# Performance work log

Measured on AMD Instinct MI355X. Metric: run time of the kernel, lower is better.

The kernel has to match this reference:

```python
import jax, jax.numpy as jnp
import numpy as np

# dims
D_MODEL = 256; D_STATE = 16; D_CONV = 4; EXPAND = 2
D_INNER = D_MODEL * EXPAND            # 512
DT_RANK = 16                          # ceil(256/16)
B_SZ = 16; C_IN = 64; T_LR = 2560; R = 2; C_OUT = 64


def _p(key, shape, scale=0.02):
    return jax.random.normal(key, shape, jnp.float32) * scale


def setup_inputs() -> dict:
    key = jax.random.key(0)
    ks = iter(jax.random.split(key, 48))
    inp = {}
    inp['x'] = jax.random.normal(next(ks), (B_SZ, C_IN, T_LR), jnp.float32)
    # encoder: Conv1d(64->128,k3,p1) ; Conv1d(128->256,k3,p1)
    inp['enc_w1'] = _p(next(ks), (128, C_IN, 3)); inp['enc_b1'] = jnp.zeros((128,), jnp.float32)
    inp['enc_w2'] = _p(next(ks), (256, 128, 3)); inp['enc_b2'] = jnp.zeros((256,), jnp.float32)
    # BidirectionalMamba norms
    inp['norm1_w'] = jnp.ones((D_MODEL,), jnp.float32)
    inp['norm2_w'] = jnp.ones((D_MODEL,), jnp.float32)
    # one forward ('f') and one backward ('b') Mamba v1 block
    for p in ('f', 'b'):
        inp[p + '_inW'] = _p(next(ks), (2 * D_INNER, D_MODEL))
        inp[p + '_convW'] = _p(next(ks), (D_INNER, D_CONV), 0.2)
        inp[p + '_convb'] = jnp.zeros((D_INNER,), jnp.float32)
        inp[p + '_xW'] = _p(next(ks), (DT_RANK + 2 * D_STATE, D_INNER))
        inp[p + '_dtW'] = _p(next(ks), (D_INNER, DT_RANK), 0.1)
        inp[p + '_dtb'] = -4.0 + 2.0 * jax.random.uniform(next(ks), (D_INNER,), jnp.float32)
        inp[p + '_Alog'] = jnp.log(jnp.tile(jnp.arange(1, D_STATE + 1, dtype=jnp.float32), (D_INNER, 1)))
        inp[p + '_D'] = jnp.ones((D_INNER,), jnp.float32)
        inp[p + '_outW'] = _p(next(ks), (D_MODEL, D_INNER))
    # post-bottleneck: Conv1d(512->256,k3,p1) + BatchNorm1d(256) (eval)
    inp['convd_w'] = _p(next(ks), (256, 512, 3)); inp['convd_b'] = jnp.zeros((256,), jnp.float32)
    inp['bn_g'] = jnp.ones((256,), jnp.float32); inp['bn_b'] = jnp.zeros((256,), jnp.float32)
    inp['bn_mean'] = jnp.zeros((256,), jnp.float32); inp['bn_var'] = jnp.ones((256,), jnp.float32)
    # SubPixel1D: Conv1d(256 -> target_channels*r, k3, p1), r=2
    inp['sp_w'] = _p(next(ks), (C_OUT * R, 256, 3)); inp['sp_b'] = jnp.zeros((C_OUT * R,), jnp.float32)
    return inp


def silu(x):
    return x * jax.nn.sigmoid(x)


def conv1d(x, w, b):  # x: (B,C,L), w: (O,I,K), 'same' padding
    k = w.shape[-1]
    y = jax.lax.conv_general_dilated(x, w, (1,), [(k // 2, k // 2)],
                                     dimension_numbers=('NCH', 'OIH', 'NCH'))
    return y + b[None, :, None]


def rmsnorm(x, w, eps=1e-6):
    return x * jax.lax.rsqrt(jnp.mean(x * x, -1, keepdims=True) + eps) * w


def mamba(x, inW, convW, convb, xW, dtW, dtb, Alog, Dp, outW):
    # x: (B, L, D_MODEL) -> (B, L, D_MODEL); Mamba v1 selective scan.
    Bn = x.shape[0]
    xz = x @ inW.T                               # (B,L,2*di)
    xc, z = jnp.split(xz, 2, axis=-1)            # (B,L,di) each
    # causal depthwise conv over time
    xt = jnp.transpose(xc, (0, 2, 1))            # (B,di,L)
    xt = jax.lax.conv_general_dilated(xt, convW[:, None, :], (1,), [(D_CONV - 1, 0)],
                                      dimension_numbers=('NCH', 'OIH', 'NCH'),
                                      feature_group_count=D_INNER)
    xc = silu(jnp.transpose(xt + convb[None, :, None], (0, 2, 1)))  # (B,L,di)
    dbc = xc @ xW.T                              # (B,L,dt_rank+2N)
    dt = jax.nn.softplus(dbc[..., :DT_RANK] @ dtW.T + dtb)          # (B,L,di)
    Bc = dbc[..., DT_RANK:DT_RANK + D_STATE]     # (B,L,N)
    Cc = dbc[..., DT_RANK + D_STATE:]            # (B,L,N)
    A = -jnp.exp(Alog)                           # (di,N)

    def step(h, inp):
        dt_t, B_t, C_t, x_t = inp                # (B,di),(B,N),(B,N),(B,di)
        dA = jnp.exp(dt_t[..., None] * A)        # (B,di,N)
        h = dA * h + (dt_t * x_t)[..., None] * B_t[:, None, :]
        y = jnp.einsum('bdn,bn->bd', h, C_t)
        return h, y

    xs = (jnp.transpose(dt, (1, 0, 2)), jnp.transpose(Bc, (1, 0, 2)),
          jnp.transpose(Cc, (1, 0, 2)), jnp.transpose(xc, (1, 0, 2)))
    h0 = jnp.zeros((Bn, D_INNER, D_STATE), x.dtype)
    _, ys = jax.lax.scan(step, h0, xs)           # ys: (L,B,di)
    y = jnp.transpose(ys, (1, 0, 2)) + xc * Dp
    return (y * silu(z)) @ outW.T


def reference(x, enc_w1, enc_b1, enc_w2, enc_b2, norm1_w, norm2_w,
              f_inW, f_convW, f_convb, f_xW, f_dtW, f_dtb, f_Alog, f_D, f_outW,
              b_inW, b_convW, b_convb, b_xW, b_dtW, b_dtb, b_Alog, b_D, b_outW,
              convd_w, convd_b, bn_g, bn_b, bn_mean, bn_var, sp_w, sp_b):
    # encoder (dropout = identity in eval)
    e = silu(conv1d(x, enc_w1, enc_b1))
    e = silu(conv1d(e, enc_w2, enc_b2))          # (B,256,T)
    t = jnp.transpose(e, (0, 2, 1))              # (B,T,256)
    # Bi-Mamba bottleneck layer
    xn = rmsnorm(t, norm1_w)
    mo_f = mamba(xn, f_inW, f_convW, f_convb, f_xW, f_dtW, f_dtb, f_Alog, f_D, f_outW) + xn
    xb = xn[:, ::-1, :]
    mo_b = mamba(xb, b_inW, b_convW, b_convb, b_xW, b_dtW, b_dtb, b_Alog, b_D, b_outW) + xb
    mo_b = mo_b[:, ::-1, :]
    combined = rmsnorm(mo_f + mo_b, norm2_w)
    m = jnp.concatenate([combined, t], axis=-1)  # (B,T,512)
    m = jnp.transpose(m, (0, 2, 1))              # (B,512,T)
    # conv_d + BatchNorm1d (eval) + SiLU
    d = conv1d(m, convd_w, convd_b)
    d = (d - bn_mean[None, :, None]) * jax.lax.rsqrt(bn_var + 1e-5)[None, :, None] \
        * bn_g[None, :, None] + bn_b[None, :, None]
    d = silu(d)
    # SubPixel1D upsample x2
    s = conv1d(d, sp_w, sp_b)                    # (B, C_OUT*R, T)
    Bn, C, T = s.shape
    s = s.reshape(Bn, C // R, R, T).transpose(0, 1, 3, 2).reshape(Bn, C // R, T * R)
    return s                                      # (B, 64, 5120)
```

## Files before the change

kernel.cpp:

```cpp
#include <hip/hip_runtime.h>
#include <hip/hip_bf16.h>
#include <math.h>

#define B_SZ 16
#define T_LR 2560
#define BT (B_SZ * T_LR)
#define DM 256
#define DI 512
#define DS 16
#define DTR 16
#define CH 128
#define CH_LOG2 7
#define CLEN (T_LR / CH)

typedef __attribute__((ext_vector_type(8))) short bf16x8;
typedef __attribute__((ext_vector_type(4))) float f32x4;

__device__ __forceinline__ float silu_f(float x) {
    return x / (1.f + __expf(-x));
}
__device__ __forceinline__ unsigned short f2bf(float v) {
    __hip_bfloat16 h = __float2bfloat16(v);
    return *(unsigned short*)&h;
}
__device__ __forceinline__ float bf2f(unsigned short u) {
    union { unsigned int i; float f; } c;
    c.i = (unsigned int)u << 16;
    return c.f;
}
__device__ __forceinline__ int seqrev(int r) {
    int s = r / T_LR, t = r % T_LR;
    return s * T_LR + (T_LR - 1 - t);
}
__device__ __forceinline__ float softplus_f(float x) {
    return (x > 20.f) ? x : __logf(1.f + __expf(x));
}

__global__ __launch_bounds__(256) void k_prep(
    const float* __restrict__ enc_w1, const float* __restrict__ enc_w2,
    const float* __restrict__ convd_w, const float* __restrict__ sp_w,
    const float* __restrict__ convd_b, const float* __restrict__ bn_g,
    const float* __restrict__ bn_b, const float* __restrict__ bn_mean,
    const float* __restrict__ bn_var,
    const float* __restrict__ inW0, const float* __restrict__ inW1,
    const float* __restrict__ outW0, const float* __restrict__ outW1,
    const float* __restrict__ xW0, const float* __restrict__ xW1,
    const float* __restrict__ Alog0, const float* __restrict__ Alog1,
    const float* __restrict__ x,
    unsigned short* __restrict__ W1r, unsigned short* __restrict__ W2r,
    unsigned short* __restrict__ Wdr, unsigned short* __restrict__ Wspr,
    float* __restrict__ alpha, float* __restrict__ beta,
    unsigned short* __restrict__ inW_bf2, unsigned short* __restrict__ outW_bf2,
    unsigned short* __restrict__ xW_bc2, float* __restrict__ Aflag,
    unsigned short* __restrict__ xt)
{
    __shared__ float ts[32][33];
    __shared__ int s_ok;
    int blk = blockIdx.x;
    int tid = threadIdx.x;
    if (blk < 32) {
        int i = blk * 256 + tid;
        int n = i / 64, ci = i % 64;
        #pragma unroll
        for (int k = 0; k < 3; k++)
            W1r[((size_t)k * 128 + n) * 64 + ci] = f2bf(enc_w1[((size_t)n * 64 + ci) * 3 + k]);
    } else if (blk < 160) {
        int i = (blk - 32) * 256 + tid;
        int n = i / 128, ci = i % 128;
        #pragma unroll
        for (int k = 0; k < 3; k++)
            W2r[((size_t)k * 256 + n) * 128 + ci] = f2bf(enc_w2[((size_t)n * 128 + ci) * 3 + k]);
    } else if (blk < 672) {
        int i = (blk - 160) * 256 + tid;
        int n = i / 512, ci = i % 512;
        #pragma unroll
        for (int k = 0; k < 3; k++)
            Wdr[((size_t)k * 256 + n) * 512 + ci] = f2bf(convd_w[((size_t)n * 512 + ci) * 3 + k]);
    } else if (blk < 800) {
        int i = (blk - 672) * 256 + tid;
        int n = i / 256, ci = i % 256;
        #pragma unroll
        for (int k = 0; k < 3; k++)
            Wspr[((size_t)k * 128 + n) * 256 + ci] = f2bf(sp_w[((size_t)n * 256 + ci) * 3 + k]);
    } else if (blk < 801) {
        int c = tid;
        float a = bn_g[c] * rsqrtf(bn_var[c] + 1e-5f);
        alpha[c] = a;
        beta[c] = (convd_b[c] - bn_mean[c]) * a + bn_b[c];
    } else if (blk < 1825) {
        int i = (blk - 801) * 256 + tid;
        inW_bf2[i] = f2bf(inW0[i]);
        inW_bf2[262144 + i] = f2bf(inW1[i]);
    } else if (blk < 2337) {
        int i = (blk - 1825) * 256 + tid;
        outW_bf2[i] = f2bf(outW0[i]);
        outW_bf2[131072 + i] = f2bf(outW1[i]);
    } else if (blk < 2433) {
        int i = (blk - 2337) * 256 + tid;
        xW_bc2[i] = f2bf(xW0[i]);
        xW_bc2[24576 + i] = f2bf(xW1[i]);
    } else if (blk < 2434) {
        if (tid == 0) s_ok = 1;
        __syncthreads();
        int ok = 1;
        for (int i = tid; i < DI * DS; i += 256) {
            int d = i >> 4, n = i & 15;
            float a0f = __expf(Alog0[d * DS]);
            float anf = __expf(Alog0[d * DS + n]);
            if (fabsf(anf - (float)(n + 1) * a0f) > 1e-3f * (float)(n + 1)) ok = 0;
            float a0b = __expf(Alog1[d * DS]);
            float anb = __expf(Alog1[d * DS + n]);
            if (fabsf(anb - (float)(n + 1) * a0b) > 1e-3f * (float)(n + 1)) ok = 0;
        }
        if (!ok) atomicAnd(&s_ok, 0);
        __syncthreads();
        if (tid == 0) Aflag[0] = s_ok ? 1.f : 0.f;
    } else {
        int idx = blk - 2434;
        int t0 = (idx % 80) * 32;
        int c0 = ((idx / 80) & 1) * 32;
        int b = idx / 160;
        int tx = tid & 31, ty = tid >> 5;
        #pragma unroll
        for (int j = 0; j < 4; j++) {
            int c = c0 + ty + j * 8;
            ts[ty + j * 8][tx] = x[((size_t)b * 64 + c) * T_LR + t0 + tx];
        }
        __syncthreads();
        #pragma unroll
        for (int j = 0; j < 4; j++) {
            int t = t0 + ty + j * 8;
            xt[((size_t)b * T_LR + t) * 64 + c0 + tx] = f2bf(ts[tx][ty + j * 8]);
        }
    }
}

__global__ __launch_bounds__(256, 4) void k_conv3_bf(const unsigned short* __restrict__ A1, int K1,
                                                  const unsigned short* __restrict__ A2, int K2,
                                                  const unsigned short* __restrict__ W,
                                                  const float* __restrict__ alpha,
                                                  const float* __restrict__ beta,
                                                  float* __restrict__ outf,
                                                  unsigned short* __restrict__ outb,
                                                  int N, int dosilu, int pixsh) {
    int Kt = K1 + K2;
    __shared__ unsigned short As[130][40];
    int tid = threadIdx.x;
    int wave = tid >> 6, lane = tid & 63;
    int wm = (wave >> 1) * 64, wn = (wave & 1) * 64;
    int m0 = blockIdx.x * 128, n0 = blockIdx.y * 128;
    int b = m0 / T_LR, t0 = m0 % T_LR;
    int q = lane >> 4, ml = lane & 15;
    const unsigned short* wbase = W + (size_t)(n0 + wn + ml) * Kt + q * 8;
    size_t tapstride = (size_t)N * Kt;
    size_t nistride  = (size_t)16 * Kt;
    f32x4 acc[4][4] = {};
    for (int k0 = 0; k0 < Kt; k0 += 32) {
        __syncthreads();
        for (int i = tid; i < 520; i += 256) {
            int row = i >> 2, cq = i & 3;
            int t = t0 - 1 + row;
            uint4 v = make_uint4(0u, 0u, 0u, 0u);
            if (t >= 0 && t < T_LR) {
                int col = k0 + cq * 8;
                const unsigned short* src = (col < K1)
                    ? A1 + (size_t)(b * T_LR + t) * K1 + col
                    : A2 + (size_t)(b * T_LR + t) * K2 + (col - K1);
                v = *(const uint4*)src;
            }
            *(uint4*)&As[row][cq * 8] = v;
        }
        __syncthreads();
        #pragma unroll
        for (int tap = 0; tap < 3; tap++) {
            bf16x8 bfr[4];
            #pragma unroll
            for (int ni = 0; ni < 4; ni++)
                bfr[ni] = *(const bf16x8*)(wbase + tap * tapstride + ni * nistride + k0);
            #pragma unroll
            for (int mi = 0; mi < 4; mi++) {
                bf16x8 af = *(const bf16x8*)&As[wm + mi * 16 + ml + tap][q * 8];
                #pragma unroll
                for (int ni = 0; ni < 4; ni++)
                    acc[mi][ni] = __builtin_amdgcn_mfma_f32_16x16x32_bf16(af, bfr[ni], acc[mi][ni], 0, 0, 0);
            }
        }
    }
    #pragma unroll
    for (int mi = 0; mi < 4; mi++) {
        #pragma unroll
        for (int r = 0; r < 4; r++) {
            int mr = m0 + wm + mi * 16 + q * 4 + r;
            int t = mr - b * T_LR;
            #pragma unroll
            for (int ni = 0; ni < 4; ni++) {
                int col = n0 + wn + ni * 16 + ml;
                float a = alpha ? alpha[col] : 1.f;
                float v = acc[mi][ni][r] * a + beta[col];
                if (dosilu) v = silu_f(v);
                if (pixsh) {
                    int c2 = col >> 1, rr = col & 1;
                    outf[(((size_t)b * 64 + c2) * T_LR + t) * 2 + rr] = v;
                } else {
                    size_t o = (size_t)mr * N + col;
                    if (outf) outf[o] = v;
                    if (outb) outb[o] = f2bf(v);
                }
            }
        }
    }
}

__global__ __launch_bounds__(256) void k_inproj_conv(const unsigned short* __restrict__ xn,
                                                     const unsigned short* __restrict__ inW,
                                                     const float* __restrict__ cw,
                                                     const float* __restrict__ cb,
                                                     unsigned short* __restrict__ xcs,
                                                     int arev) {
    __shared__ unsigned short As[128][40];
    __shared__ unsigned short Bs[128][40];
    __shared__ unsigned short Ct[131][136];
    int tid = threadIdx.x;
    int wave = tid >> 6, lane = tid & 63;
    int wm = (wave >> 1) * 64, wn = (wave & 1) * 64;
    int m0 = blockIdx.x * 128, n0 = blockIdx.y * 128;
    int b = m0 / T_LR, t0 = m0 % T_LR;
    int sc = tid & 3, sr = tid >> 2;
    int ar0 = m0 + sr, ar1 = m0 + sr + 64;
    if (arev) { ar0 = seqrev(ar0); ar1 = seqrev(ar1); }
    const unsigned short* ap0 = xn + (size_t)ar0 * DM + sc * 8;
    const unsigned short* ap1 = xn + (size_t)ar1 * DM + sc * 8;
    const unsigned short* bp0 = inW + (size_t)(n0 + sr) * DM + sc * 8;
    const unsigned short* bp1 = inW + (size_t)(n0 + sr + 64) * DM + sc * 8;
    f32x4 acc[4][4] = {};
    int q = lane >> 4, ml = lane & 15;
    for (int k0 = 0; k0 < DM; k0 += 32) {
        uint4 a0 = *(const uint4*)(ap0 + k0);
        uint4 a1 = *(const uint4*)(ap1 + k0);
        uint4 b0 = *(const uint4*)(bp0 + k0);
        uint4 b1 = *(const uint4*)(bp1 + k0);
        __syncthreads();
        *(uint4*)&As[sr][sc * 8]      = a0;
        *(uint4*)&As[sr + 64][sc * 8] = a1;
        *(uint4*)&Bs[sr][sc * 8]      = b0;
        *(uint4*)&Bs[sr + 64][sc * 8] = b1;
        __syncthreads();
        bf16x8 af[4], bfr[4];
        #pragma unroll
        for (int mi = 0; mi < 4; mi++)
            af[mi] = *(const bf16x8*)&As[wm + mi * 16 + ml][q * 8];
        #pragma unroll
        for (int ni = 0; ni < 4; ni++)
            bfr[ni] = *(const bf16x8*)&Bs[wn + ni * 16 + ml][q * 8];
        #pragma unroll
        for (int mi = 0; mi < 4; mi++)
            #pragma unroll
            for (int ni = 0; ni < 4; ni++)
                acc[mi][ni] = __builtin_amdgcn_mfma_f32_16x16x32_bf16(af[mi], bfr[ni], acc[mi][ni], 0, 0, 0);
    }
    #pragma unroll
    for (int mi = 0; mi < 4; mi++)
        #pragma unroll
        for (int r = 0; r < 4; r++)
            #pragma unroll
            for (int ni = 0; ni < 4; ni++)
                Ct[3 + wm + mi * 16 + q * 4 + r][wn + ni * 16 + ml] = f2bf(acc[mi][ni][r]);
    for (int i = tid; i < 384; i += 256) {
        int hr = i >> 7, c = i & 127;
        int tr = t0 - 3 + hr;
        float v = 0.f;
        if (tr >= 0) {
            int src = b * T_LR + (arev ? (T_LR - 1 - tr) : tr);
            const unsigned short* xr = xn + (size_t)src * DM;
            const unsigned short* wr = inW + (size_t)(n0 + c) * DM;
            for (int k = 0; k < DM; k += 8) {
                uint4 xa = *(const uint4*)(xr + k);
                uint4 wa = *(const uint4*)(wr + k);
                const unsigned short* xs = (const unsigned short*)&xa;
                const unsigned short* wsp = (const unsigned short*)&wa;
                #pragma unroll
                for (int j = 0; j < 8; j++) v += bf2f(xs[j]) * bf2f(wsp[j]);
            }
        }
        Ct[hr][c] = f2bf(v);
    }
    __syncthreads();
    int col = tid & 127;
    int d = n0 + col;
    float w0 = cw[d * 4 + 0], w1 = cw[d * 4 + 1], w2 = cw[d * 4 + 2], w3 = cw[d * 4 + 3];
    float bi = cb[d];
    int rbase = tid >> 7;
    for (int j = 0; j < 64; j++) {
        int row = rbase + 2 * j;
        float v = bi + bf2f(Ct[row][col]) * w0 + bf2f(Ct[row + 1][col]) * w1
                     + bf2f(Ct[row + 2][col]) * w2 + bf2f(Ct[row + 3][col]) * w3;
        xcs[(size_t)(m0 + row) * DI + d] = f2bf(silu_f(v));
    }
}

__global__ __launch_bounds__(256) void k_rmsnorm(const float* __restrict__ in1,
                                                 const float* __restrict__ w,
                                                 float* __restrict__ out,
                                                 unsigned short* __restrict__ out_bf,
                                                 int ntok) {
    int tok = (blockIdx.x * 256 + threadIdx.x) >> 6;
    int lane = threadIdx.x & 63;
    if (tok >= ntok) return;
    float4 v = ((const float4*)(in1 + (size_t)tok * DM))[lane];
    float ss = v.x * v.x + v.y * v.y + v.z * v.z + v.w * v.w;
    #pragma unroll
    for (int off = 32; off > 0; off >>= 1) ss += __shfl_xor(ss, off);
    float sc = rsqrtf(ss * (1.f / 256.f) + 1e-6f);
    float4 wv = ((const float4*)w)[lane];
    float4 o;
    o.x = v.x * sc * wv.x; o.y = v.y * sc * wv.y;
    o.z = v.z * sc * wv.z; o.w = v.w * sc * wv.w;
    if (out) ((float4*)(out + (size_t)tok * DM))[lane] = o;
    if (out_bf) {
        ushort4 ob;
        ob.x = f2bf(o.x); ob.y = f2bf(o.y); ob.z = f2bf(o.z); ob.w = f2bf(o.w);
        ((ushort4*)(out_bf + (size_t)tok * DM))[lane] = ob;
    }
}

__global__ __launch_bounds__(256) void k_gemm_bf(const unsigned short* __restrict__ A, int lda,
                                                 const unsigned short* __restrict__ Bw,
                                                 float* Cf, unsigned short* Cb, int ldc,
                                                 const float* __restrict__ res,
                                                 const float* __restrict__ bias,
                                                 const unsigned short* __restrict__ gate,
                                                 int K, int Nout, int act,
                                                 int arev, int crev, int accum) {
    __shared__ unsigned short As[128][40];
    __shared__ unsigned short Bs[128][40];
    int tid = threadIdx.x;
    int wave = tid >> 6, lane = tid & 63;
    int wm = (wave >> 1) * 64, wn = (wave & 1) * 64;
    int m0 = blockIdx.x * 128, n0 = blockIdx.y * 128;
    int sc = tid & 3, sr = tid >> 2;
    int ar0 = m0 + sr, ar1 = m0 + sr + 64;
    if (arev) { ar0 = seqrev(ar0); ar1 = seqrev(ar1); }
    const unsigned short* ap0 = A + (size_t)ar0 * lda + sc * 8;
    const unsigned short* ap1 = A + (size_t)ar1 * lda + sc * 8;
    bool bv0 = (n0 + sr) < Nout;
    bool bv1 = (n0 + sr + 64) < Nout;
    const unsigned short* bp0 = Bw + (size_t)(n0 + sr) * K + sc * 8;
    const unsigned short* bp1 = Bw + (size_t)(n0 + sr + 64) * K + sc * 8;
    f32x4 acc[4][4] = {};
    int q = lane >> 4, ml = lane & 15;
    for (int k0 = 0; k0 < K; k0 += 32) {
        uint4 a0 = *(const uint4*)(ap0 + k0);
        uint4 a1 = *(const uint4*)(ap1 + k0);
        uint4 b0 = make_uint4(0u, 0u, 0u, 0u), b1 = make_uint4(0u, 0u, 0u, 0u);
        if (bv0) b0 = *(const uint4*)(bp0 + k0);
        if (bv1) b1 = *(const uint4*)(bp1 + k0);
        __syncthreads();
        *(uint4*)&As[sr][sc * 8]      = a0;
        *(uint4*)&As[sr + 64][sc * 8] = a1;
        *(uint4*)&Bs[sr][sc * 8]      = b0;
        *(uint4*)&Bs[sr + 64][sc * 8] = b1;
        __syncthreads();
        bf16x8 af[4], bfr[4];
        #pragma unroll
        for (int mi = 0; mi < 4; mi++)
            af[mi] = *(const bf16x8*)&As[wm + mi * 16 + ml][q * 8];
        #pragma unroll
        for (int ni = 0; ni < 4; ni++)
            bfr[ni] = *(const bf16x8*)&Bs[wn + ni * 16 + ml][q * 8];
        #pragma unroll
        for (int mi = 0; mi < 4; mi++)
            #pragma unroll
            for (int ni = 0; ni < 4; ni++)
                acc[mi][ni] = __builtin_amdgcn_mfma_f32_16x16x32_bf16(af[mi], bfr[ni], acc[mi][ni], 0, 0, 0);
    }
    #pragma unroll
    for (int mi = 0; mi < 4; mi++) {
        #pragma unroll
        for (int r = 0; r < 4; r++) {
            int mr = m0 + wm + mi * 16 + q * 4 + r;
            int orow = crev ? seqrev(mr) : mr;
            #pragma unroll
            for (int ni = 0; ni < 4; ni++) {
                int col = n0 + wn + ni * 16 + ml;
                if (col < Nout) {
                    float v = acc[mi][ni][r];
                    if (bias) v += bias[col];
                    if (act == 2) v = softplus_f(v);
                    if (gate) v = silu_f(v) * bf2f(gate[(size_t)mr * ldc + col]);
                    if (res) v += res[(size_t)orow * ldc + col];
                    if (accum) v += Cf[(size_t)orow * ldc + col];
                    if (Cf) Cf[(size_t)orow * ldc + col] = v;
                    if (Cb) Cb[(size_t)orow * ldc + col] = f2bf(v);
                }
            }
        }
    }
}

__global__ __launch_bounds__(256) void k_gemm_bf_cb(const unsigned short* __restrict__ A, int lda,
                                                    const unsigned short* __restrict__ Bw,
                                                    unsigned short* __restrict__ Cb, int ldc,
                                                    const float* __restrict__ bias,
                                                    const unsigned short* __restrict__ gate,
                                                    int K, int act, int arev) {
    __shared__ __align__(16) unsigned short smem[2 * 128 * 40];
    unsigned short (*As)[40] = (unsigned short(*)[40])smem;
    unsigned short (*Bs)[40] = (unsigned short(*)[40])(smem + 128 * 40);
    float* sC = (float*)smem;
    int tid = threadIdx.x;
    int wave = tid >> 6, lane = tid & 63;
    int wm = (wave >> 1) * 64, wn = (wave & 1) * 64;
    int m0 = blockIdx.x * 128, n0 = blockIdx.y * 128;
    int sc = tid & 3, sr = tid >> 2;
    int ar0 = m0 + sr, ar1 = m0 + sr + 64;
    if (arev) { ar0 = seqrev(ar0); ar1 = seqrev(ar1); }
    const unsigned short* ap0 = A + (size_t)ar0 * lda + sc * 8;
    const unsigned short* ap1 = A + (size_t)ar1 * lda + sc * 8;
    const unsigned short* bp0 = Bw + (size_t)(n0 + sr) * K + sc * 8;
    const unsigned short* bp1 = Bw + (size_t)(n0 + sr + 64) * K + sc * 8;
    f32x4 acc[4][4] = {};
    int q = lane >> 4, ml = lane & 15;
    for (int k0 = 0; k0 < K; k0 += 32) {
        uint4 a0 = *(const uint4*)(ap0 + k0);
        uint4 a1 = *(const uint4*)(ap1 + k0);
        uint4 b0 = *(const uint4*)(bp0 + k0);
        uint4 b1 = *(const uint4*)(bp1 + k0);
        __syncthreads();
        *(uint4*)&As[sr][sc * 8]      = a0;
        *(uint4*)&As[sr + 64][sc * 8] = a1;
        *(uint4*)&Bs[sr][sc * 8]      = b0;
        *(uint4*)&Bs[sr + 64][sc * 8] = b1;
        __syncthreads();
        bf16x8 af[4], bfr[4];
        #pragma unroll
        for (int mi = 0; mi < 4; mi++)
            af[mi] = *(const bf16x8*)&As[wm + mi * 16 + ml][q * 8];
        #pragma unroll
        for (int ni = 0; ni < 4; ni++)
            bfr[ni] = *(const bf16x8*)&Bs[wn + ni * 16 + ml][q * 8];
        #pragma unroll
        for (int mi = 0; mi < 4; mi++)
            #pragma unroll
            for (int ni = 0; ni < 4; ni++)
                acc[mi][ni] = __builtin_amdgcn_mfma_f32_16x16x32_bf16(af[mi], bfr[ni], acc[mi][ni], 0, 0, 0);
    }
    #pragma unroll
    for (int p = 0; p < 4; p++) {
        __syncthreads();
        if ((wave >> 1) == (p >> 1)) {
            int mib = (p & 1) * 2;
            #pragma unroll
            for (int m2 = 0; m2 < 2; m2++) {
                int mi = mib + m2;
                int rl = mi * 16 + q * 4 - (p & 1) * 32;
                #pragma unroll
                for (int r = 0; r < 4; r++)
                    #pragma unroll
                    for (int ni = 0; ni < 4; ni++)
                        sC[(rl + r) * 140 + wn + ni * 16 + ml] = acc[mi][ni][r];
            }
        }
        __syncthreads();
        #pragma unroll
        for (int gi = 0; gi < 2; gi++) {
            int g = tid + gi * 256;
            int row = g >> 4;
            int colg = (g & 15) * 8;
            int grow = m0 + p * 32 + row;
            const float* src = sC + row * 140 + colg;
            float4 v0 = *(const float4*)src;
            float4 v1 = *(const float4*)(src + 4);
            float vv[8] = {v0.x, v0.y, v0.z, v0.w, v1.x, v1.y, v1.z, v1.w};
            unsigned short gu[8];
            if (gate)
                *(uint4*)gu = *(const uint4*)(gate + (size_t)grow * ldc + n0 + colg);
            unsigned short o[8];
            #pragma unroll
            for (int jj = 0; jj < 8; jj++) {
                float v = vv[jj];
                if (bias) v += bias[n0 + colg + jj];
                if (act == 2) v = softplus_f(v);
                if (gate) v = silu_f(v) * bf2f(gu[jj]);
                o[jj] = f2bf(v);
            }
            *(uint4*)(Cb + (size_t)grow * ldc + n0 + colg) = *(uint4*)o;
        }
    }
}

__global__ __launch_bounds__(256) void k_scan_p1(const unsigned short* __restrict__ x,
                                                 const float* __restrict__ db,
                                                 const float* __restrict__ dtW,
                                                 const float* __restrict__ dtb,
                                                 const float* __restrict__ Alog,
                                                 const float* __restrict__ Aflag,
                                                 float* __restrict__ hS,
                                                 float* __restrict__ csum) {
    __shared__ float dbs[CLEN * 48];
    int tid = threadIdx.x;
    int gid = blockIdx.x * 256 + tid;
    int d = gid & (DI - 1);
    int bcix = gid >> 9;
    int c = bcix & (CH - 1);
    int bl = bcix >> CH_LOG2;
    int tbase = c * CLEN;
    const float* dbp = db + ((size_t)bl * T_LR + tbase) * 48;
    if (tid < 240) *(float4*)&dbs[tid * 4] = *(const float4*)(dbp + tid * 4);
    bool fast = (Aflag[0] != 0.f);
    float A0 = -__expf(Alog[d * DS]);
    float Av[DS], h[DS];
    #pragma unroll
    for (int n = 0; n < DS; n++) h[n] = 0.f;
    if (!fast) {
        #pragma unroll
        for (int n = 0; n < DS; n++) Av[n] = -__expf(Alog[d * DS + n]);
    }
    const float4* wp = (const float4*)(dtW + d * 16);
    float4 w0 = wp[0], w1 = wp[1], w2 = wp[2], w3 = wp[3];
    float bias = dtb[d];
    const unsigned short* xp = x + ((size_t)bl * T_LR + tbase) * DI + d;
    float S = 0.f;
    __syncthreads();
    for (int t = 0; t < CLEN; t++) {
        const float* bc = dbs + t * 48;
        float dl = bias
            + bc[0] * w0.x + bc[1] * w0.y + bc[2] * w0.z + bc[3] * w0.w
            + bc[4] * w1.x + bc[5] * w1.y + bc[6] * w1.z + bc[7] * w1.w
            + bc[8] * w2.x + bc[9] * w2.y + bc[10] * w2.z + bc[11] * w2.w
            + bc[12] * w3.x + bc[13] * w3.y + bc[14] * w3.z + bc[15] * w3.w;
        float dtv = softplus_f(dl);
        float xv  = bf2f(xp[(size_t)t * DI]);
        float dtx = dtv * xv;
        S += dtv;
        if (fast) {
            float e1 = __expf(dtv * A0);
            float e = e1;
            #pragma unroll
            for (int n = 0; n < DS; n++) {
                h[n] = e * h[n] + dtx * bc[16 + n];
                e *= e1;
            }
        } else {
            #pragma unroll
            for (int n = 0; n < DS; n++)
                h[n] = __expf(dtv * Av[n]) * h[n] + dtx * bc[16 + n];
        }
    }
    float* hp = hS + (size_t)gid * DS;
    #pragma unroll
    for (int n = 0; n < DS; n++) hp[n] = h[n];
    csum[gid] = S;
}

__global__ __launch_bounds__(256) void k_scan_p2(float* __restrict__ hS,
                                                 const float* __restrict__ csum,
                                                 const float* __restrict__ Alog) {
    int gid = blockIdx.x * 256 + threadIdx.x;
    int n = gid & (DS - 1);
    int d = (gid >> 4) & (DI - 1);
    int bl = gid >> 13;
    float An = -__expf(Alog[d * DS + n]);
    float hs = 0.f;
    for (int c = 0; c < CH; c++) {
        size_t base = ((size_t)(bl * CH + c) * DI + d);
        float he = hS[base * DS + n];
        float S  = csum[base];
        hS[base * DS + n] = hs;
        hs = __expf(An * S) * hs + he;
    }
}

__global__ __launch_bounds__(256) void k_scan_p3(unsigned short* __restrict__ x,
                                                 const float* __restrict__ db,
                                                 const float* __restrict__ dtW,
                                                 const float* __restrict__ dtb,
                                                 const float* __restrict__ Alog,
                                                 const float* __restrict__ Aflag,
                                                 const float* __restrict__ Dp,
                                                 const float* __restrict__ hS) {
    __shared__ float dbs[CLEN * 48];
    int tid = threadIdx.x;
    int gid = blockIdx.x * 256 + tid;
    int d = gid & (DI - 1);
    int bcix = gid >> 9;
    int c = bcix & (CH - 1);
    int bl = bcix >> CH_LOG2;
    int tbase = c * CLEN;
    const float* dbp = db + ((size_t)bl * T_LR + tbase) * 48;
    if (tid < 240) *(float4*)&dbs[tid * 4] = *(const float4*)(dbp + tid * 4);
    bool fast = (Aflag[0] != 0.f);
    float A0 = -__expf(Alog[d * DS]);
    float Av[DS], h[DS];
    const float* hp = hS + (size_t)gid * DS;
    #pragma unroll
    for (int n = 0; n < DS; n++) h[n] = hp[n];
    if (!fast) {
        #pragma unroll
        for (int n = 0; n < DS; n++) Av[n] = -__expf(Alog[d * DS + n]);
    }
    const float4* wp = (const float4*)(dtW + d * 16);
    float4 w0 = wp[0], w1 = wp[1], w2 = wp[2], w3 = wp[3];
    float bias = dtb[d];
    float Dd = Dp[d];
    unsigned short* xp = x + ((size_t)bl * T_LR + tbase) * DI + d;
    __syncthreads();
    for (int t = 0; t < CLEN; t++) {
        const float* bc = dbs + t * 48;
        float dl = bias
            + bc[0] * w0.x + bc[1] * w0.y + bc[2] * w0.z + bc[3] * w0.w
            + bc[4] * w1.x + bc[5] * w1.y + bc[6] * w1.z + bc[7] * w1.w
            + bc[8] * w2.x + bc[9] * w2.y + bc[10] * w2.z + bc[11] * w2.w
            + bc[12] * w3.x + bc[13] * w3.y + bc[14] * w3.z + bc[15] * w3.w;
        float dtv = softplus_f(dl);
        float xv  = bf2f(xp[(size_t)t * DI]);
        float dtx = dtv * xv;
        float acc = 0.f;
        if (fast) {
            float e1 = __expf(dtv * A0);
            float e = e1;
            #pragma unroll
            for (int n = 0; n < DS; n++) {
                h[n] = e * h[n] + dtx * bc[16 + n];
                acc += h[n] * bc[32 + n];
                e *= e1;
            }
        } else {
            #pragma unroll
            for (int n = 0; n < DS; n++) {
                h[n] = __expf(dtv * Av[n]) * h[n] + dtx * bc[16 + n];
                acc += h[n] * bc[32 + n];
            }
        }
        xp[(size_t)t * DI] = f2bf(acc + xv * Dd);
    }
}

extern "C" void kernel_launch(void* const* d_in, const int* in_sizes, int n_in,
                              void* d_out, int out_size, void* d_ws, size_t ws_size,
                              hipStream_t stream) {
    const float* x       = (const float*)d_in[0];
    const float* enc_w1  = (const float*)d_in[1];
    const float* enc_b1  = (const float*)d_in[2];
    const float* enc_w2  = (const float*)d_in[3];
    const float* enc_b2  = (const float*)d_in[4];
    const float* norm1_w = (const float*)d_in[5];
    const float* norm2_w = (const float*)d_in[6];
    const float* convd_w = (const float*)d_in[25];
    const float* convd_b = (const float*)d_in[26];
    const float* bn_g    = (const float*)d_in[27];
    const float* bn_b    = (const float*)d_in[28];
    const float* bn_mean = (const float*)d_in[29];
    const float* bn_var  = (const float*)d_in[30];
    const float* sp_w    = (const float*)d_in[31];
    const float* sp_b    = (const float*)d_in[32];
    float* out = (float*)d_out;

    const float* inW0   = (const float*)d_in[7];
    const float* xW0    = (const float*)d_in[10];
    const float* outW0  = (const float*)d_in[15];
    const float* inW1   = (const float*)d_in[16];
    const float* xW1    = (const float*)d_in[19];
    const float* outW1  = (const float*)d_in[24];
    const float* Alog0  = (const float*)d_in[13];
    const float* Alog1  = (const float*)d_in[22];

    float* ws = (float*)d_ws;
    size_t availf = ws_size / sizeof(float);
    size_t o = 0;
    float* t_buf  = ws + o; o += (size_t)BT * DM;
    float* xn_buf = ws + o; o += (size_t)BT * DM;
    float* mo     = ws + o; o += (size_t)BT * DM;
    unsigned short* xn_bf = (unsigned short*)(ws + o); o += (size_t)BT * DM / 2;
    unsigned short* tb_bf = (unsigned short*)(ws + o); o += (size_t)BT * DM / 2;
    unsigned short* inW_bf2  = (unsigned short*)(ws + o); o += (size_t)1024 * DM;
    unsigned short* outW_bf2 = (unsigned short*)(ws + o); o += (size_t)DM * DI;
    unsigned short* xW_bc2   = (unsigned short*)(ws + o); o += (size_t)48 * DI;
    unsigned short* W1r  = (unsigned short*)(ws + o); o += (3 * 128 * 64) / 2;
    unsigned short* W2r  = (unsigned short*)(ws + o); o += (3 * 256 * 128) / 2;
    unsigned short* Wdr  = (unsigned short*)(ws + o); o += (3 * 256 * 512) / 2;
    unsigned short* Wspr = (unsigned short*)(ws + o); o += (3 * 128 * 256) / 2;
    float* alpha_d = ws + o; o += 256;
    float* beta_d  = ws + o; o += 256;
    float* Aflag_d = ws + o; o += 4;
    size_t persist = o;
    float* scratch = ws + persist;
    size_t scratch_avail = (availf > persist) ? (availf - persist) : 0;
    size_t per_b = (size_t)T_LR * DI / 2 * 2 + (size_t)T_LR * 48
                 + (size_t)CH * DI * (DS + 1);
    int Bc = 16;
    while (Bc > 1 && (size_t)Bc * per_b > scratch_avail) Bc >>= 1;

    unsigned short* xt  = (unsigned short*)mo;
    unsigned short* e1t = (unsigned short*)(mo + (size_t)BT * 64 / 2);
    unsigned short* comb_bf = (unsigned short*)xn_buf;
    unsigned short* d_bf = (unsigned short*)mo;

    k_prep<<<4994, 256, 0, stream>>>(enc_w1, enc_w2, convd_w, sp_w,
                                     convd_b, bn_g, bn_b, bn_mean, bn_var,
                                     inW0, inW1, outW0, outW1, xW0, xW1,
                                     Alog0, Alog1,
                                     x, W1r, W2r, Wdr, Wspr, alpha_d, beta_d,
                                     inW_bf2, outW_bf2, xW_bc2, Aflag_d, xt);

    k_conv3_bf<<<dim3(BT / 128, 1), 256, 0, stream>>>(xt, 64, nullptr, 0, W1r,
                                                      nullptr, enc_b1, nullptr, e1t, 128, 1, 0);
    k_conv3_bf<<<dim3(BT / 128, 2), 256, 0, stream>>>(e1t, 128, nullptr, 0, W2r,
                                                      nullptr, enc_b2, t_buf, tb_bf, 256, 1, 0);
    k_rmsnorm<<<BT / 4, 256, 0, stream>>>(t_buf, norm1_w, xn_buf, xn_bf, BT);

    for (int dir = 0; dir < 2; dir++) {
        const float* convW = (const float*)d_in[8 + 9 * dir];
        const float* convb = (const float*)d_in[9 + 9 * dir];
        const float* dtW   = (const float*)d_in[11 + 9 * dir];
        const float* dtb   = (const float*)d_in[12 + 9 * dir];
        const float* Alog  = (const float*)d_in[13 + 9 * dir];
        const float* Dp    = (const float*)d_in[14 + 9 * dir];
        const unsigned short* inW_d  = inW_bf2 + (size_t)dir * 1024 * DM;
        const unsigned short* outW_d = outW_bf2 + (size_t)dir * DM * DI;
        const unsigned short* xWbc_d = xW_bc2 + (size_t)dir * 48 * DI;
        int rev = dir;
        for (int b0 = 0; b0 < B_SZ; b0 += Bc) {
            int Tc = Bc * T_LR;
            unsigned short* xcs = (unsigned short*)scratch;
            unsigned short* ygb = xcs + (size_t)Tc * DI;
            float* db   = (float*)(ygb + (size_t)Tc * DI);
            float* hS   = db + (size_t)Tc * 48;
            float* csum = hS + (size_t)Bc * CH * DI * DS;
            const float*          xnC  = xn_buf + (size_t)b0 * T_LR * DM;
            const unsigned short* xnbC = xn_bf  + (size_t)b0 * T_LR * DM;
            float*                moC  = mo     + (size_t)b0 * T_LR * DM;
            k_inproj_conv<<<dim3(Tc / 128, DI / 128), 256, 0, stream>>>(
                xnbC, inW_d, convW, convb, xcs, rev);
            k_gemm_bf<<<dim3(Tc / 128, 1), 256, 0, stream>>>(
                xcs, DI, xWbc_d, db, nullptr, 48, nullptr, nullptr, nullptr,
                DI, 48, 0, 0, 0, 0);
            k_scan_p1<<<(Bc * CH * DI) / 256, 256, 0, stream>>>(xcs, db, dtW, dtb, Alog, Aflag_d, hS, csum);
            k_scan_p2<<<(Bc * DI * DS) / 256, 256, 0, stream>>>(hS, csum, Alog);
            k_scan_p3<<<(Bc * CH * DI) / 256, 256, 0, stream>>>(xcs, db, dtW, dtb, Alog, Aflag_d, Dp, hS);
            k_gemm_bf_cb<<<dim3(Tc / 128, DI / 128), 256, 0, stream>>>(
                xnbC, DM, inW_d + (size_t)DI * DM, ygb, DI, nullptr, xcs, DM, 0, rev);
            k_gemm_bf<<<dim3(Tc / 128, DM / 128), 256, 0, stream>>>(
                ygb, DI, outW_d, moC, nullptr, DM, xnC, nullptr, nullptr,
                DI, DM, 0, 0, rev, dir);
        }
    }

    k_rmsnorm<<<BT / 4, 256, 0, stream>>>(mo, norm2_w, nullptr, comb_bf, BT);
    k_conv3_bf<<<dim3(BT / 128, 2), 256, 0, stream>>>(comb_bf, 256, tb_bf, 256, Wdr,
                                                      alpha_d, beta_d, nullptr, d_bf, 256, 1, 0);
    k_conv3_bf<<<dim3(BT / 128, 1), 256, 0, stream>>>(d_bf, 256, nullptr, 0, Wspr,
                                                      nullptr, sp_b, out, nullptr, 128, 0, 1);
}
```

Measured before the change: 1.320 ms.

## Double-buffer conv3 LDS tiles and halve the M tile to 64 rows

The conv3 GEMM kernel now uses two LDS buffers. The next K-slice of activations is loaded into registers while MFMAs run on the current slice, and is written to the other buffer afterwards, which removes one barrier per iteration. The M tile shrinks from 128 to 64 rows per block, so the grid doubles and each wave computes 2x4 instead of 4x4 MFMA tiles. This trades more weight reloads per output and less reuse for better latency hiding and occupancy.

```diff
diff --git a/kernel.cpp b/kernel.cpp
--- a/kernel.cpp
+++ b/kernel.cpp
@@ -144,33 +144,66 @@
                                                   unsigned short* __restrict__ outb,
                                                   int N, int dosilu, int pixsh) {
     int Kt = K1 + K2;
-    __shared__ unsigned short As[130][40];
+    __shared__ unsigned short As[2][66][40];
     int tid = threadIdx.x;
     int wave = tid >> 6, lane = tid & 63;
-    int wm = (wave >> 1) * 64, wn = (wave & 1) * 64;
-    int m0 = blockIdx.x * 128, n0 = blockIdx.y * 128;
+    int wm = (wave >> 1) * 32, wn = (wave & 1) * 64;
+    int m0 = blockIdx.x * 64, n0 = blockIdx.y * 128;
     int b = m0 / T_LR, t0 = m0 % T_LR;
     int q = lane >> 4, ml = lane & 15;
     const unsigned short* wbase = W + (size_t)(n0 + wn + ml) * Kt + q * 8;
     size_t tapstride = (size_t)N * Kt;
     size_t nistride  = (size_t)16 * Kt;
-    f32x4 acc[4][4] = {};
-    for (int k0 = 0; k0 < Kt; k0 += 32) {
-        __syncthreads();
-        for (int i = tid; i < 520; i += 256) {
-            int row = i >> 2, cq = i & 3;
-            int t = t0 - 1 + row;
-            uint4 v = make_uint4(0u, 0u, 0u, 0u);
-            if (t >= 0 && t < T_LR) {
-                int col = k0 + cq * 8;
+    f32x4 acc[2][4] = {};
+    int row0 = tid >> 2, cq0 = tid & 3;
+    int row1 = (tid + 256) >> 2, cq1 = tid & 3;
+    bool has1 = (tid + 256) < 264;
+    int ta = t0 - 1 + row0;
+    int tb = t0 - 1 + row1;
+    bool va = (ta >= 0 && ta < T_LR);
+    bool vb = has1 && (tb >= 0 && tb < T_LR);
+    uint4 v0 = make_uint4(0u, 0u, 0u, 0u), v1 = make_uint4(0u, 0u, 0u, 0u);
+    {
+        int col = cq0 * 8;
+        if (va) {
+            const unsigned short* src = (col < K1)
+                ? A1 + (size_t)(b * T_LR + ta) * K1 + col
+                : A2 + (size_t)(b * T_LR + ta) * K2 + (col - K1);
+            v0 = *(const uint4*)src;
+        }
+        if (vb) {
+            int col1 = cq1 * 8;
+            const unsigned short* src = (col1 < K1)
+                ? A1 + (size_t)(b * T_LR + tb) * K1 + col1
+                : A2 + (size_t)(b * T_LR + tb) * K2 + (col1 - K1);
+            v1 = *(const uint4*)src;
+        }
+        *(uint4*)&As[0][row0][cq0 * 8] = v0;
+        if (has1) *(uint4*)&As[0][row1][cq1 * 8] = v1;
+    }
+    int nk = Kt >> 5;
+    for (int kk = 0; kk < nk; kk++) {
+        __syncthreads();
+        int cur = kk & 1;
+        int k0 = kk << 5;
+        if (kk + 1 < nk) {
+            int col = k0 + 32 + cq0 * 8;
+            v0 = make_uint4(0u, 0u, 0u, 0u);
+            v1 = make_uint4(0u, 0u, 0u, 0u);
+            if (va) {
                 const unsigned short* src = (col < K1)
-                    ? A1 + (size_t)(b * T_LR + t) * K1 + col
-                    : A2 + (size_t)(b * T_LR + t) * K2 + (col - K1);
-                v = *(const uint4*)src;
-            }
-            *(uint4*)&As[row][cq * 8] = v;
-        }
-        __syncthreads();
+                    ? A1 + (size_t)(b * T_LR + ta) * K1 + col
+                    : A2 + (size_t)(b * T_LR + ta) * K2 + (col - K1);
+                v0 = *(const uint4*)src;
+            }
+            if (vb) {
+                int col1 = k0 + 32 + cq1 * 8;
+                const unsigned short* src = (col1 < K1)
+                    ? A1 + (size_t)(b * T_LR + tb) * K1 + col1
+                    : A2 + (size_t)(b * T_LR + tb) * K2 + (col1 - K1);
+                v1 = *(const uint4*)src;
+            }
+        }
         #pragma unroll
         for (int tap = 0; tap < 3; tap++) {
             bf16x8 bfr[4];
@@ -178,16 +211,20 @@
             for (int ni = 0; ni < 4; ni++)
                 bfr[ni] = *(const bf16x8*)(wbase + tap * tapstride + ni * nistride + k0);
             #pragma unroll
-            for (int mi = 0; mi < 4; mi++) {
-                bf16x8 af = *(const bf16x8*)&As[wm + mi * 16 + ml + tap][q * 8];
+            for (int mi = 0; mi < 2; mi++) {
+                bf16x8 af = *(const bf16x8*)&As[cur][wm + mi * 16 + ml + tap][q * 8];
                 #pragma unroll
                 for (int ni = 0; ni < 4; ni++)
                     acc[mi][ni] = __builtin_amdgcn_mfma_f32_16x16x32_bf16(af, bfr[ni], acc[mi][ni], 0, 0, 0);
             }
         }
+        if (kk + 1 < nk) {
+            *(uint4*)&As[cur ^ 1][row0][cq0 * 8] = v0;
+            if (has1) *(uint4*)&As[cur ^ 1][row1][cq1 * 8] = v1;
+        }
     }
     #pragma unroll
-    for (int mi = 0; mi < 4; mi++) {
+    for (int mi = 0; mi < 2; mi++) {
         #pragma unroll
         for (int r = 0; r < 4; r++) {
             int mr = m0 + wm + mi * 16 + q * 4 + r;
@@ -702,9 +739,9 @@
                                      x, W1r, W2r, Wdr, Wspr, alpha_d, beta_d,
                                      inW_bf2, outW_bf2, xW_bc2, Aflag_d, xt);
 
-    k_conv3_bf<<<dim3(BT / 128, 1), 256, 0, stream>>>(xt, 64, nullptr, 0, W1r,
+    k_conv3_bf<<<dim3(BT / 64, 1), 256, 0, stream>>>(xt, 64, nullptr, 0, W1r,
                                                       nullptr, enc_b1, nullptr, e1t, 128, 1, 0);
-    k_conv3_bf<<<dim3(BT / 128, 2), 256, 0, stream>>>(e1t, 128, nullptr, 0, W2r,
+    k_conv3_bf<<<dim3(BT / 64, 2), 256, 0, stream>>>(e1t, 128, nullptr, 0, W2r,
                                                       nullptr, enc_b2, t_buf, tb_bf, 256, 1, 0);
     k_rmsnorm<<<BT / 4, 256, 0, stream>>>(t_buf, norm1_w, xn_buf, xn_bf, BT);
 
@@ -746,8 +783,8 @@
     }
 
     k_rmsnorm<<<BT / 4, 256, 0, stream>>>(mo, norm2_w, nullptr, comb_bf, BT);
-    k_conv3_bf<<<dim3(BT / 128, 2), 256, 0, stream>>>(comb_bf, 256, tb_bf, 256, Wdr,
+    k_conv3_bf<<<dim3(BT / 64, 2), 256, 0, stream>>>(comb_bf, 256, tb_bf, 256, Wdr,
                                                       alpha_d, beta_d, nullptr, d_bf, 256, 1, 0);
-    k_conv3_bf<<<dim3(BT / 128, 1), 256, 0, stream>>>(d_bf, 256, nullptr, 0, Wspr,
+    k_conv3_bf<<<dim3(BT / 64, 1), 256, 0, stream>>>(d_bf, 256, nullptr, 0, Wspr,
                                                       nullptr, sp_b, out, nullptr, 128, 0, 1);
 }
```

Measured after the change: 1.397 ms. +5.8%, slower.

## Double-buffer LDS activation tile in conv3 GEMM with register prefetch

Applied to the files above, without the earlier changes.

Converts the conv3 bf16 MFMA kernel's K-loop to a double-buffered shared-memory scheme. The next K-slice of activations is loaded into registers before the MFMAs run and written to the alternate buffer afterwards, which removes one barrier per iteration and overlaps global loads with compute. In exchange, shared memory doubles, more registers are live, and launch bounds drop from 4 to 3 blocks per CU, which may reduce occupancy.

```diff
diff --git a/kernel.cpp b/kernel.cpp
--- a/kernel.cpp
+++ b/kernel.cpp
@@ -135,7 +135,7 @@
     }
 }
 
-__global__ __launch_bounds__(256, 4) void k_conv3_bf(const unsigned short* __restrict__ A1, int K1,
+__global__ __launch_bounds__(256, 3) void k_conv3_bf(const unsigned short* __restrict__ A1, int K1,
                                                   const unsigned short* __restrict__ A2, int K2,
                                                   const unsigned short* __restrict__ W,
                                                   const float* __restrict__ alpha,
@@ -144,7 +144,7 @@
                                                   unsigned short* __restrict__ outb,
                                                   int N, int dosilu, int pixsh) {
     int Kt = K1 + K2;
-    __shared__ unsigned short As[130][40];
+    __shared__ unsigned short As[2][130][40];
     int tid = threadIdx.x;
     int wave = tid >> 6, lane = tid & 63;
     int wm = (wave >> 1) * 64, wn = (wave & 1) * 64;
@@ -155,22 +155,38 @@
     size_t tapstride = (size_t)N * Kt;
     size_t nistride  = (size_t)16 * Kt;
     f32x4 acc[4][4] = {};
-    for (int k0 = 0; k0 < Kt; k0 += 32) {
-        __syncthreads();
-        for (int i = tid; i < 520; i += 256) {
-            int row = i >> 2, cq = i & 3;
-            int t = t0 - 1 + row;
-            uint4 v = make_uint4(0u, 0u, 0u, 0u);
-            if (t >= 0 && t < T_LR) {
-                int col = k0 + cq * 8;
-                const unsigned short* src = (col < K1)
-                    ? A1 + (size_t)(b * T_LR + t) * K1 + col
-                    : A2 + (size_t)(b * T_LR + t) * K2 + (col - K1);
-                v = *(const uint4*)src;
-            }
-            *(uint4*)&As[row][cq * 8] = v;
-        }
-        __syncthreads();
+    int cq = tid & 3;
+    int r0 = tid >> 2;
+    int r1 = r0 + 64;
+    int r2 = r0 + 128;
+    bool has2 = (tid < 8);
+    int ta0 = t0 - 1 + r0, ta1 = t0 - 1 + r1, ta2 = t0 - 1 + r2;
+    bool va0 = (ta0 >= 0) && (ta0 < T_LR);
+    bool va1 = (ta1 < T_LR);
+    bool va2 = has2 && (ta2 < T_LR);
+    uint4 v0, v1, v2;
+    #define LOADA(vv, valid, t, col) { vv = make_uint4(0u,0u,0u,0u); if (valid) { \
+        const unsigned short* src = ((col) < K1) \
+            ? A1 + (size_t)(b * T_LR + (t)) * K1 + (col) \
+            : A2 + (size_t)(b * T_LR + (t)) * K2 + ((col) - K1); \
+        vv = *(const uint4*)src; } }
+    LOADA(v0, va0, ta0, cq * 8);
+    LOADA(v1, va1, ta1, cq * 8);
+    LOADA(v2, va2, ta2, cq * 8);
+    *(uint4*)&As[0][r0][cq * 8] = v0;
+    *(uint4*)&As[0][r1][cq * 8] = v1;
+    if (has2) *(uint4*)&As[0][r2][cq * 8] = v2;
+    int nk = Kt >> 5;
+    for (int kk = 0; kk < nk; kk++) {
+        __syncthreads();
+        int cur = kk & 1;
+        int k0 = kk << 5;
+        if (kk + 1 < nk) {
+            int col = k0 + 32 + cq * 8;
+            LOADA(v0, va0, ta0, col);
+            LOADA(v1, va1, ta1, col);
+            LOADA(v2, va2, ta2, col);
+        }
         #pragma unroll
         for (int tap = 0; tap < 3; tap++) {
             bf16x8 bfr[4];
@@ -179,13 +195,19 @@
                 bfr[ni] = *(const bf16x8*)(wbase + tap * tapstride + ni * nistride + k0);
             #pragma unroll
             for (int mi = 0; mi < 4; mi++) {
-                bf16x8 af = *(const bf16x8*)&As[wm + mi * 16 + ml + tap][q * 8];
+                bf16x8 af = *(const bf16x8*)&As[cur][wm + mi * 16 + ml + tap][q * 8];
                 #pragma unroll
                 for (int ni = 0; ni < 4; ni++)
                     acc[mi][ni] = __builtin_amdgcn_mfma_f32_16x16x32_bf16(af, bfr[ni], acc[mi][ni], 0, 0, 0);
             }
         }
-    }
+        if (kk + 1 < nk) {
+            *(uint4*)&As[cur ^ 1][r0][cq * 8] = v0;
+            *(uint4*)&As[cur ^ 1][r1][cq * 8] = v1;
+            if (has2) *(uint4*)&As[cur ^ 1][r2][cq * 8] = v2;
+        }
+    }
+    #undef LOADA
     #pragma unroll
     for (int mi = 0; mi < 4; mi++) {
         #pragma unroll
```

Measured after the change: 1.318 ms. About the same (-0.1%).
